# Kernel optimization log

Hardware: AMD Instinct MI355X
Metric: run time of the kernel (lower is better)

## Reference

```python
import jax, jax.numpy as jnp
import numpy as np

HIDDEN = 4096
NH = 32        # query heads
HD = 128       # head dim
NKV = 8        # kv heads
RD = 64        # rotary dim (partial rotary)
THETA = 10000.0
SEQ = 2048


def _rope(x, positions):
    # x: [S, H, HD]; neox-style rope on first RD dims of each head
    half = RD // 2
    inv_freq = 1.0 / (THETA ** (jnp.arange(half, dtype=jnp.float32) / half))
    freqs = positions.astype(jnp.float32)[:, None] * inv_freq[None, :]  # [S, half]
    cos = jnp.cos(freqs)[:, None, :]  # [S,1,half]
    sin = jnp.sin(freqs)[:, None, :]
    x_rot, x_pass = x[..., :RD], x[..., RD:]
    x1, x2 = x_rot[..., :half], x_rot[..., half:]
    o1 = x1 * cos - x2 * sin
    o2 = x2 * cos + x1 * sin
    return jnp.concatenate([o1, o2, x_pass], axis=-1)


def setup_inputs() -> dict:
    key = jax.random.key(0)
    k1, k2, k3 = jax.random.split(key, 3)
    hidden_states = jax.random.normal(k1, (SEQ, HIDDEN), dtype=jnp.float32)
    Wqkv = jax.random.normal(k2, (HIDDEN, (NH + 2 * NKV) * HD), dtype=jnp.float32) * 0.02
    Wo = jax.random.normal(k3, (NH * HD, HIDDEN), dtype=jnp.float32) * 0.02
    positions = jnp.arange(SEQ, dtype=jnp.int64)
    return {"hidden_states": hidden_states, "Wqkv": Wqkv, "Wo": Wo, "positions": positions}


def reference(hidden_states, Wqkv, Wo, positions):
    S = hidden_states.shape[0]
    qkv = hidden_states @ Wqkv  # [S, (NH+2*NKV)*HD]
    q, k, v = jnp.split(qkv, [NH * HD, NH * HD + NKV * HD], axis=-1)
    q = q.reshape(S, NH, HD)
    k = k.reshape(S, NKV, HD)
    v = v.reshape(S, NKV, HD)
    q = _rope(q, positions)
    k = _rope(k, positions)
    # GQA: expand kv heads to query heads
    g = NH // NKV
    k = jnp.repeat(k, g, axis=1)  # [S, NH, HD]
    v = jnp.repeat(v, g, axis=1)
    scale = HD ** -0.5
    scores = jnp.einsum('shd,thd->hst', q, k) * scale  # [NH, S, S]
    causal = jnp.tril(jnp.ones((S, S), dtype=bool))
    scores = jnp.where(causal[None, :, :], scores, jnp.finfo(scores.dtype).min)
    probs = jax.nn.softmax(scores, axis=-1)
    attn = jnp.einsum('hst,thd->shd', probs, v).reshape(S, NH * HD)
    return attn @ Wo
```

## Files before the change

### kernel.cpp

```cpp
#include <hip/hip_runtime.h>

#define S_LEN 2048
#define HID 4096
#define NH 32
#define NKV 8
#define HD 128
#define QKVN 6144
#define KOFF 4096
#define VOFF 5120

typedef unsigned short ushort_t;
typedef unsigned int uint_t;
typedef __attribute__((ext_vector_type(8))) short short8;
typedef __attribute__((ext_vector_type(4))) short short4v;
typedef __attribute__((ext_vector_type(4))) float float4_t;

__device__ __forceinline__ float bf2f(ushort_t u) {
    return __uint_as_float(((uint_t)u) << 16);
}
__device__ __forceinline__ uint_t f2bf(float f) {
    uint_t u = __float_as_uint(f);
    u += 0x7fffu + ((u >> 16) & 1u);
    return u >> 16;
}

__device__ __forceinline__ void gload_lds16(const ushort_t* g, ushort_t* l) {
    __builtin_amdgcn_global_load_lds(
        (const __attribute__((address_space(1))) void*)g,
        (__attribute__((address_space(3))) void*)l, 16, 0, 0);
}

__global__ void f32_to_bf16(const float* __restrict__ in,
                            ushort_t* __restrict__ out) {
    int i = blockIdx.x * 256 + threadIdx.x;
    out[i] = (ushort_t)f2bf(in[i]);
}

__global__ void transpose_f32_bf16(const float* __restrict__ in,
                                   ushort_t* __restrict__ out, int R, int C) {
    __shared__ float t[32][33];
    int c0 = blockIdx.x * 32, r0 = blockIdx.y * 32;
    int ci = threadIdx.x & 31, rb = threadIdx.x >> 5;
#pragma unroll
    for (int p = 0; p < 4; p++) {
        int ri = rb + p * 8;
        t[ri][ci] = in[(size_t)(r0 + ri) * C + c0 + ci];
    }
    __syncthreads();
#pragma unroll
    for (int p = 0; p < 4; p++) {
        int ri = rb + p * 8;
        out[(size_t)(c0 + ri) * R + r0 + ci] = (ushort_t)f2bf(t[ci][ri]);
    }
}

__global__ __launch_bounds__(256, 2)
void gemm_bf16(const ushort_t* __restrict__ A, const ushort_t* __restrict__ BT,
               float* __restrict__ Cout, int M, int N, int K) {
    __shared__ __attribute__((aligned(16))) ushort_t As[128 * 32];
    __shared__ __attribute__((aligned(16))) ushort_t Bs[128 * 32];
    const int tid  = threadIdx.x;
    const int wave = tid >> 6;
    const int lane = tid & 63;
    const int quad = lane >> 4;
    const int l16  = lane & 15;
    const int m0 = blockIdx.y * 128;
    const int n0 = blockIdx.x * 128;
    const int wm = (wave & 1) * 64;
    const int wn = (wave >> 1) * 64;

    const int r0 = tid >> 2;
    const int kc = (tid & 3) * 8;
    const ushort_t* gA0 = A  + (size_t)(m0 + r0)      * K + kc;
    const ushort_t* gA1 = A  + (size_t)(m0 + r0 + 64) * K + kc;
    const ushort_t* gB0 = BT + (size_t)(n0 + r0)      * K + kc;
    const ushort_t* gB1 = BT + (size_t)(n0 + r0 + 64) * K + kc;
    ushort_t* lA0 = &As[r0 * 32 + kc];
    ushort_t* lA1 = lA0 + 64 * 32;
    ushort_t* lB0 = &Bs[r0 * 32 + kc];
    ushort_t* lB1 = lB0 + 64 * 32;

    float4_t acc[4][4] = {};

    for (int k0 = 0; k0 < K; k0 += 32) {
        gload_lds16(gA0 + k0, lA0);
        gload_lds16(gA1 + k0, lA1);
        gload_lds16(gB0 + k0, lB0);
        gload_lds16(gB1 + k0, lB1);
        __syncthreads();

        short8 af[4], bfr[4];
#pragma unroll
        for (int i = 0; i < 4; i++)
            af[i] = *(const short8*)(&As[(wm + i * 16 + l16) * 32 + quad * 8]);
#pragma unroll
        for (int j = 0; j < 4; j++)
            bfr[j] = *(const short8*)(&Bs[(wn + j * 16 + l16) * 32 + quad * 8]);
#pragma unroll
        for (int i = 0; i < 4; i++)
#pragma unroll
            for (int j = 0; j < 4; j++)
                acc[i][j] = __builtin_amdgcn_mfma_f32_16x16x32_bf16(
                    af[i], bfr[j], acc[i][j], 0, 0, 0);
        __syncthreads();
    }

#pragma unroll
    for (int i = 0; i < 4; i++)
#pragma unroll
        for (int j = 0; j < 4; j++)
#pragma unroll
            for (int r = 0; r < 4; r++) {
                int row = m0 + wm + i * 16 + quad * 4 + r;
                int col = n0 + wn + j * 16 + l16;
                Cout[(size_t)row * N + col] = acc[i][j][r];
            }
}

#define QSC 0.12753102543918255f
__global__ void prep_q(const float* __restrict__ qkv, ushort_t* __restrict__ Qb) {
    int idx = blockIdx.x * 256 + threadIdx.x;
    int d = idx & 127;
    int s = (idx >> 7) & 2047;
    int h = idx >> 18;
    const float* row = qkv + (size_t)s * QKVN + h * HD;
    float v;
    if (d < 64) {
        int i = d & 31;
        float invf = exp2f(-(float)i * (13.287712379549449f / 32.0f));
        float fr = (float)s * invf;
        float c, sn;
        sincosf(fr, &sn, &c);
        float x1 = row[i], x2 = row[i + 32];
        v = (d < 32) ? (x1 * c - x2 * sn) : (x2 * c + x1 * sn);
    } else {
        v = row[d];
    }
    Qb[idx] = (ushort_t)f2bf(v * QSC);
}

__global__ void prep_k(const float* __restrict__ qkv, ushort_t* __restrict__ Kb) {
    int idx = blockIdx.x * 256 + threadIdx.x;
    int d = idx & 127;
    int t = (idx >> 7) & 2047;
    int hk = idx >> 18;
    const float* row = qkv + (size_t)t * QKVN + KOFF + hk * HD;
    float v;
    if (d < 64) {
        int i = d & 31;
        float invf = exp2f(-(float)i * (13.287712379549449f / 32.0f));
        float fr = (float)t * invf;
        float c, sn;
        sincosf(fr, &sn, &c);
        float x1 = row[i], x2 = row[i + 32];
        v = (d < 32) ? (x1 * c - x2 * sn) : (x2 * c + x1 * sn);
    } else {
        v = row[d];
    }
    Kb[idx] = (ushort_t)f2bf(v);
}

__global__ void prep_v(const float* __restrict__ qkv, ushort_t* __restrict__ Vt) {
    __shared__ float tile[32][33];
    int hk = blockIdx.z;
    int t0 = blockIdx.x * 32, d0 = blockIdx.y * 32;
    int ci = threadIdx.x & 31, rb = threadIdx.x >> 5;
#pragma unroll
    for (int p = 0; p < 4; p++) {
        int tr = rb + p * 8;
        tile[tr][ci] = qkv[(size_t)(t0 + tr) * QKVN + VOFF + hk * HD + d0 + ci];
    }
    __syncthreads();
#pragma unroll
    for (int p = 0; p < 4; p++) {
        int dr = rb + p * 8;
        Vt[((size_t)hk * HD + d0 + dr) * S_LEN + t0 + ci] = (ushort_t)f2bf(tile[ci][dr]);
    }
}

__global__ __launch_bounds__(256, 4)
void flash_attn(const ushort_t* __restrict__ Qb, const ushort_t* __restrict__ Kb,
                const ushort_t* __restrict__ Vt, ushort_t* __restrict__ attn) {
    __shared__ __attribute__((aligned(16))) ushort_t Ks[2][32 * 128];
    __shared__ __attribute__((aligned(16))) ushort_t Vs[2][128 * 32];

    const int h    = blockIdx.y;
    const int hk   = h >> 2;
    const int tid  = threadIdx.x;
    const int wave = tid >> 6;
    const int lane = tid & 63;
    const int quad = lane >> 4;
    const int l16  = lane & 15;
    const int bx   = 31 - (int)blockIdx.x;
    const int qt   = 4 * bx + wave;
    const int qw   = qt * 16;

    const ushort_t* Qh = Qb + (size_t)h  * S_LEN * HD;
    const ushort_t* Kh = Kb + (size_t)hk * S_LEN * HD;
    const ushort_t* Vh = Vt + (size_t)hk * HD * S_LEN;

    const int krow = tid >> 4;
    const int ksrc = ((tid & 15) ^ (krow & 7)) << 3;
    const ushort_t* gK0 = Kh + (size_t)krow * HD + ksrc;
    const ushort_t* gK1 = Kh + (size_t)(krow + 16) * HD + ksrc;
    const int vrow = tid >> 2;
    const int vtb  = (tid & 3) << 3;
    const ushort_t* gV0 = Vh + (size_t)vrow * S_LEN + vtb;
    const ushort_t* gV1 = Vh + (size_t)(vrow + 64) * S_LEN + vtb;

    ushort_t* lK = &Ks[0][tid * 8];
    ushort_t* lV = &Vs[0][tid * 8];

#define STAGE(buf, t0)                                                        \
    do {                                                                      \
        gload_lds16(gK0 + (size_t)(t0) * HD, lK + (buf) * (32 * 128));        \
        gload_lds16(gK1 + (size_t)(t0) * HD, lK + (buf) * (32 * 128) + 2048); \
        gload_lds16(gV0 + (t0),              lV + (buf) * (128 * 32));        \
        gload_lds16(gV1 + (t0),              lV + (buf) * (128 * 32) + 2048); \
    } while (0)

    short8 qf[4];
#pragma unroll
    for (int c = 0; c < 4; c++)
        qf[c] = *(const short8*)(Qh + (size_t)(qw + l16) * HD + c * 32 + quad * 8);

    float4_t oacc[8] = {};
    float lsum = 0.f;
    const int s0 = (((quad * 2)     & 3) << 4) | l16;
    const int s1 = (((quad * 2 + 1) & 3) << 4) | l16;

    const int T0w   = qw & ~31;
    const int T0max = (16 * (4 * bx + 3)) & ~31;
    const int kxor  = (l16 & 7) << 3;

    STAGE(0, 0);
    __syncthreads();

#pragma unroll 1
    for (int t0 = 0; t0 <= T0max; t0 += 32) {
        const int cur = (t0 >> 5) & 1;
        if (t0 + 32 <= T0max) STAGE(cur ^ 1, t0 + 32);

        const ushort_t* Kbuf = Ks[cur];
        const ushort_t* Vbuf = Vs[cur];

        float4_t stA = {}, stB = {};
#pragma unroll
        for (int c = 0; c < 4; c++) {
            short8 kfA = *(const short8*)(Kbuf + l16 * 128 +
                                          ((c * 32 + quad * 8) ^ kxor));
            short8 kfB = *(const short8*)(Kbuf + (16 + l16) * 128 +
                                          ((c * 32 + quad * 8) ^ kxor));
            stA = __builtin_amdgcn_mfma_f32_16x16x32_bf16(kfA, qf[c], stA, 0, 0, 0);
            stB = __builtin_amdgcn_mfma_f32_16x16x32_bf16(kfB, qf[c], stB, 0, 0, 0);
        }

        const bool maskT = (t0 >= T0w);
        float pA[4], pB[4];
#pragma unroll
        for (int r = 0; r < 4; r++) {
            float eA = exp2f(stA[r]);
            float eB = exp2f(stB[r]);
            if (maskT) {
                int tA = t0 + quad * 4 + r;
                eA = (tA      <= qw + l16) ? eA : 0.f;
                eB = (tA + 16 <= qw + l16) ? eB : 0.f;
            }
            pA[r] = eA; pB[r] = eB;
            lsum += eA + eB;
        }

        uint_t a01 = f2bf(pA[0]) | (f2bf(pA[1]) << 16);
        uint_t a23 = f2bf(pA[2]) | (f2bf(pA[3]) << 16);
        uint_t b01 = f2bf(pB[0]) | (f2bf(pB[1]) << 16);
        uint_t b23 = f2bf(pB[2]) | (f2bf(pB[3]) << 16);
        uint_t A01s0 = (uint_t)__shfl((int)a01, s0);
        uint_t A23s0 = (uint_t)__shfl((int)a23, s0);
        uint_t B01s0 = (uint_t)__shfl((int)b01, s0);
        uint_t B23s0 = (uint_t)__shfl((int)b23, s0);
        uint_t A01s1 = (uint_t)__shfl((int)a01, s1);
        uint_t A23s1 = (uint_t)__shfl((int)a23, s1);
        uint_t B01s1 = (uint_t)__shfl((int)b01, s1);
        uint_t B23s1 = (uint_t)__shfl((int)b23, s1);
        uint_t w[4];
        w[0] = quad < 2 ? A01s0 : B01s0;
        w[1] = quad < 2 ? A23s0 : B23s0;
        w[2] = quad < 2 ? A01s1 : B01s1;
        w[3] = quad < 2 ? A23s1 : B23s1;
        short8 pb;
        __builtin_memcpy(&pb, w, 16);

#pragma unroll
        for (int dt = 0; dt < 8; dt++) {
            short8 vf = *(const short8*)(Vbuf + (dt * 16 + l16) * 32 + quad * 8);
            oacc[dt] = __builtin_amdgcn_mfma_f32_16x16x32_bf16(vf, pb, oacc[dt], 0, 0, 0);
        }

        __syncthreads();
    }
#undef STAGE

    lsum += __shfl_xor(lsum, 16);
    lsum += __shfl_xor(lsum, 32);
    float invl = 1.f / lsum;
    ushort_t* orow = attn + (size_t)(qw + l16) * (NH * HD) + h * HD;
#pragma unroll
    for (int dt = 0; dt < 8; dt++) {
        short4v wv;
#pragma unroll
        for (int r = 0; r < 4; r++)
            wv[r] = (short)f2bf(oacc[dt][r] * invl);
        *(short4v*)(orow + dt * 16 + quad * 4) = wv;
    }
}

extern "C" void kernel_launch(void* const* d_in, const int* in_sizes, int n_in,
                              void* d_out, int out_size, void* d_ws, size_t ws_size,
                              hipStream_t stream) {
    const float* hidden = (const float*)d_in[0];
    const float* Wqkv   = (const float*)d_in[1];
    const float* Wo     = (const float*)d_in[2];
    float* out = (float*)d_out;

    char* ws = (char*)d_ws;
    float*    qkv   = (float*)   (ws);
    ushort_t* attnB = (ushort_t*)(ws);
    ushort_t* hidB  = (ushort_t*)(ws + 50331648);
    ushort_t* Qb    = hidB;
    ushort_t* WqkvT = (ushort_t*)(ws + 67108864);
    ushort_t* WoT   = (ushort_t*)(ws + 117440512);
    ushort_t* Kb    = (ushort_t*)(ws + 150994944);
    ushort_t* Vt    = (ushort_t*)(ws + 155189248);

    f32_to_bf16<<<(S_LEN * HID) / 256, 256, 0, stream>>>(hidden, hidB);
    transpose_f32_bf16<<<dim3(QKVN / 32, HID / 32), 256, 0, stream>>>(Wqkv, WqkvT, HID, QKVN);
    transpose_f32_bf16<<<dim3(HID / 32, HID / 32), 256, 0, stream>>>(Wo, WoT, HID, HID);

    gemm_bf16<<<dim3(QKVN / 128, S_LEN / 128), 256, 0, stream>>>(
        hidB, WqkvT, qkv, S_LEN, QKVN, HID);

    prep_q<<<(NH  * S_LEN * HD) / 256, 256, 0, stream>>>(qkv, Qb);
    prep_k<<<(NKV * S_LEN * HD) / 256, 256, 0, stream>>>(qkv, Kb);
    prep_v<<<dim3(S_LEN / 32, HD / 32, NKV), 256, 0, stream>>>(qkv, Vt);

    flash_attn<<<dim3(32, NH), 256, 0, stream>>>(Qb, Kb, Vt, attnB);

    gemm_bf16<<<dim3(HID / 128, S_LEN / 128), 256, 0, stream>>>(
        attnB, WoT, out, S_LEN, HID, HID);
}
```

Measured before the change: 590.1 us.

## Vectorize conversions, precompute rope table, interleave causal query tiles in attention

Vectorizes the hidden-state bf16 conversion to float4 loads and packs two bf16 values per store in the weight transpose. Adds a cos/sin rope table kernel so prep_q/prep_k stop recomputing sincos per element. Reassigns query tiles in flash attention so each block's waves hold tiles 32 apart, balancing causal work across blocks, and skips tiles beyond each wave's diagonal. The trade-off is that waves within a block now diverge in loop length while still sharing the K/V loads and barriers.

```diff
diff --git a/kernel.cpp b/kernel.cpp
--- a/kernel.cpp
+++ b/kernel.cpp
@@ -30,10 +30,16 @@
         (__attribute__((address_space(3))) void*)l, 16, 0, 0);
 }
 
-__global__ void f32_to_bf16(const float* __restrict__ in,
-                            ushort_t* __restrict__ out) {
+__global__ void f32_to_bf16(const float4* __restrict__ in,
+                            short4v* __restrict__ out) {
     int i = blockIdx.x * 256 + threadIdx.x;
-    out[i] = (ushort_t)f2bf(in[i]);
+    float4 v = in[i];
+    short4v o;
+    o[0] = (short)f2bf(v.x);
+    o[1] = (short)f2bf(v.y);
+    o[2] = (short)f2bf(v.z);
+    o[3] = (short)f2bf(v.w);
+    out[i] = o;
 }
 
 __global__ void transpose_f32_bf16(const float* __restrict__ in,
@@ -47,10 +53,13 @@
         t[ri][ci] = in[(size_t)(r0 + ri) * C + c0 + ci];
     }
     __syncthreads();
-#pragma unroll
-    for (int p = 0; p < 4; p++) {
-        int ri = rb + p * 8;
-        out[(size_t)(c0 + ri) * R + r0 + ci] = (ushort_t)f2bf(t[ci][ri]);
+    int cp = (threadIdx.x & 15) * 2;
+    int rw = threadIdx.x >> 4;
+#pragma unroll
+    for (int p = 0; p < 2; p++) {
+        int ri = rw + p * 16;
+        uint_t w = f2bf(t[cp][ri]) | (f2bf(t[cp + 1][ri]) << 16);
+        *(uint_t*)(&out[(size_t)(c0 + ri) * R + r0 + cp]) = w;
     }
 }
 
@@ -117,8 +126,20 @@
             }
 }
 
+__global__ void rope_tab_k(float2* __restrict__ tab) {
+    int idx = blockIdx.x * 256 + threadIdx.x;
+    int i = idx & 31;
+    int s = idx >> 5;
+    float invf = exp2f(-(float)i * (13.287712379549449f / 32.0f));
+    float fr = (float)s * invf;
+    float c, sn;
+    sincosf(fr, &sn, &c);
+    tab[idx] = make_float2(c, sn);
+}
+
 #define QSC 0.12753102543918255f
-__global__ void prep_q(const float* __restrict__ qkv, ushort_t* __restrict__ Qb) {
+__global__ void prep_q(const float* __restrict__ qkv, const float2* __restrict__ tab,
+                       ushort_t* __restrict__ Qb) {
     int idx = blockIdx.x * 256 + threadIdx.x;
     int d = idx & 127;
     int s = (idx >> 7) & 2047;
@@ -127,19 +148,17 @@
     float v;
     if (d < 64) {
         int i = d & 31;
-        float invf = exp2f(-(float)i * (13.287712379549449f / 32.0f));
-        float fr = (float)s * invf;
-        float c, sn;
-        sincosf(fr, &sn, &c);
+        float2 cs = tab[(s << 5) + i];
         float x1 = row[i], x2 = row[i + 32];
-        v = (d < 32) ? (x1 * c - x2 * sn) : (x2 * c + x1 * sn);
+        v = (d < 32) ? (x1 * cs.x - x2 * cs.y) : (x2 * cs.x + x1 * cs.y);
     } else {
         v = row[d];
     }
     Qb[idx] = (ushort_t)f2bf(v * QSC);
 }
 
-__global__ void prep_k(const float* __restrict__ qkv, ushort_t* __restrict__ Kb) {
+__global__ void prep_k(const float* __restrict__ qkv, const float2* __restrict__ tab,
+                       ushort_t* __restrict__ Kb) {
     int idx = blockIdx.x * 256 + threadIdx.x;
     int d = idx & 127;
     int t = (idx >> 7) & 2047;
@@ -148,12 +167,9 @@
     float v;
     if (d < 64) {
         int i = d & 31;
-        float invf = exp2f(-(float)i * (13.287712379549449f / 32.0f));
-        float fr = (float)t * invf;
-        float c, sn;
-        sincosf(fr, &sn, &c);
+        float2 cs = tab[(t << 5) + i];
         float x1 = row[i], x2 = row[i + 32];
-        v = (d < 32) ? (x1 * c - x2 * sn) : (x2 * c + x1 * sn);
+        v = (d < 32) ? (x1 * cs.x - x2 * cs.y) : (x2 * cs.x + x1 * cs.y);
     } else {
         v = row[d];
     }
@@ -191,8 +207,8 @@
     const int lane = tid & 63;
     const int quad = lane >> 4;
     const int l16  = lane & 15;
-    const int bx   = 31 - (int)blockIdx.x;
-    const int qt   = 4 * bx + wave;
+    const int bx   = (int)blockIdx.x;
+    const int qt   = bx + 32 * wave;
     const int qw   = qt * 16;
 
     const ushort_t* Qh = Qb + (size_t)h  * S_LEN * HD;
@@ -230,7 +246,7 @@
     const int s1 = (((quad * 2 + 1) & 3) << 4) | l16;
 
     const int T0w   = qw & ~31;
-    const int T0max = (16 * (4 * bx + 3)) & ~31;
+    const int T0max = ((bx + 96) * 16) & ~31;
     const int kxor  = (l16 & 7) << 3;
 
     STAGE(0, 0);
@@ -241,59 +257,61 @@
         const int cur = (t0 >> 5) & 1;
         if (t0 + 32 <= T0max) STAGE(cur ^ 1, t0 + 32);
 
-        const ushort_t* Kbuf = Ks[cur];
-        const ushort_t* Vbuf = Vs[cur];
-
-        float4_t stA = {}, stB = {};
-#pragma unroll
-        for (int c = 0; c < 4; c++) {
-            short8 kfA = *(const short8*)(Kbuf + l16 * 128 +
-                                          ((c * 32 + quad * 8) ^ kxor));
-            short8 kfB = *(const short8*)(Kbuf + (16 + l16) * 128 +
-                                          ((c * 32 + quad * 8) ^ kxor));
-            stA = __builtin_amdgcn_mfma_f32_16x16x32_bf16(kfA, qf[c], stA, 0, 0, 0);
-            stB = __builtin_amdgcn_mfma_f32_16x16x32_bf16(kfB, qf[c], stB, 0, 0, 0);
-        }
-
-        const bool maskT = (t0 >= T0w);
-        float pA[4], pB[4];
-#pragma unroll
-        for (int r = 0; r < 4; r++) {
-            float eA = exp2f(stA[r]);
-            float eB = exp2f(stB[r]);
-            if (maskT) {
-                int tA = t0 + quad * 4 + r;
-                eA = (tA      <= qw + l16) ? eA : 0.f;
-                eB = (tA + 16 <= qw + l16) ? eB : 0.f;
+        if (t0 <= T0w) {
+            const ushort_t* Kbuf = Ks[cur];
+            const ushort_t* Vbuf = Vs[cur];
+
+            float4_t stA = {}, stB = {};
+#pragma unroll
+            for (int c = 0; c < 4; c++) {
+                short8 kfA = *(const short8*)(Kbuf + l16 * 128 +
+                                              ((c * 32 + quad * 8) ^ kxor));
+                short8 kfB = *(const short8*)(Kbuf + (16 + l16) * 128 +
+                                              ((c * 32 + quad * 8) ^ kxor));
+                stA = __builtin_amdgcn_mfma_f32_16x16x32_bf16(kfA, qf[c], stA, 0, 0, 0);
+                stB = __builtin_amdgcn_mfma_f32_16x16x32_bf16(kfB, qf[c], stB, 0, 0, 0);
             }
-            pA[r] = eA; pB[r] = eB;
-            lsum += eA + eB;
-        }
-
-        uint_t a01 = f2bf(pA[0]) | (f2bf(pA[1]) << 16);
-        uint_t a23 = f2bf(pA[2]) | (f2bf(pA[3]) << 16);
-        uint_t b01 = f2bf(pB[0]) | (f2bf(pB[1]) << 16);
-        uint_t b23 = f2bf(pB[2]) | (f2bf(pB[3]) << 16);
-        uint_t A01s0 = (uint_t)__shfl((int)a01, s0);
-        uint_t A23s0 = (uint_t)__shfl((int)a23, s0);
-        uint_t B01s0 = (uint_t)__shfl((int)b01, s0);
-        uint_t B23s0 = (uint_t)__shfl((int)b23, s0);
-        uint_t A01s1 = (uint_t)__shfl((int)a01, s1);
-        uint_t A23s1 = (uint_t)__shfl((int)a23, s1);
-        uint_t B01s1 = (uint_t)__shfl((int)b01, s1);
-        uint_t B23s1 = (uint_t)__shfl((int)b23, s1);
-        uint_t w[4];
-        w[0] = quad < 2 ? A01s0 : B01s0;
-        w[1] = quad < 2 ? A23s0 : B23s0;
-        w[2] = quad < 2 ? A01s1 : B01s1;
-        w[3] = quad < 2 ? A23s1 : B23s1;
-        short8 pb;
-        __builtin_memcpy(&pb, w, 16);
-
-#pragma unroll
-        for (int dt = 0; dt < 8; dt++) {
-            short8 vf = *(const short8*)(Vbuf + (dt * 16 + l16) * 32 + quad * 8);
-            oacc[dt] = __builtin_amdgcn_mfma_f32_16x16x32_bf16(vf, pb, oacc[dt], 0, 0, 0);
+
+            const bool maskT = (t0 == T0w);
+            float pA[4], pB[4];
+#pragma unroll
+            for (int r = 0; r < 4; r++) {
+                float eA = exp2f(stA[r]);
+                float eB = exp2f(stB[r]);
+                if (maskT) {
+                    int tA = t0 + quad * 4 + r;
+                    eA = (tA      <= qw + l16) ? eA : 0.f;
+                    eB = (tA + 16 <= qw + l16) ? eB : 0.f;
+                }
+                pA[r] = eA; pB[r] = eB;
+                lsum += eA + eB;
+            }
+
+            uint_t a01 = f2bf(pA[0]) | (f2bf(pA[1]) << 16);
+            uint_t a23 = f2bf(pA[2]) | (f2bf(pA[3]) << 16);
+            uint_t b01 = f2bf(pB[0]) | (f2bf(pB[1]) << 16);
+            uint_t b23 = f2bf(pB[2]) | (f2bf(pB[3]) << 16);
+            uint_t A01s0 = (uint_t)__shfl((int)a01, s0);
+            uint_t A23s0 = (uint_t)__shfl((int)a23, s0);
+            uint_t B01s0 = (uint_t)__shfl((int)b01, s0);
+            uint_t B23s0 = (uint_t)__shfl((int)b23, s0);
+            uint_t A01s1 = (uint_t)__shfl((int)a01, s1);
+            uint_t A23s1 = (uint_t)__shfl((int)a23, s1);
+            uint_t B01s1 = (uint_t)__shfl((int)b01, s1);
+            uint_t B23s1 = (uint_t)__shfl((int)b23, s1);
+            uint_t w[4];
+            w[0] = quad < 2 ? A01s0 : B01s0;
+            w[1] = quad < 2 ? A23s0 : B23s0;
+            w[2] = quad < 2 ? A01s1 : B01s1;
+            w[3] = quad < 2 ? A23s1 : B23s1;
+            short8 pb;
+            __builtin_memcpy(&pb, w, 16);
+
+#pragma unroll
+            for (int dt = 0; dt < 8; dt++) {
+                short8 vf = *(const short8*)(Vbuf + (dt * 16 + l16) * 32 + quad * 8);
+                oacc[dt] = __builtin_amdgcn_mfma_f32_16x16x32_bf16(vf, pb, oacc[dt], 0, 0, 0);
+            }
         }
 
         __syncthreads();
@@ -328,19 +346,22 @@
     ushort_t* hidB  = (ushort_t*)(ws + 50331648);
     ushort_t* Qb    = hidB;
     ushort_t* WqkvT = (ushort_t*)(ws + 67108864);
+    float2*   rtab  = (float2*)  (ws + 67108864);
     ushort_t* WoT   = (ushort_t*)(ws + 117440512);
     ushort_t* Kb    = (ushort_t*)(ws + 150994944);
     ushort_t* Vt    = (ushort_t*)(ws + 155189248);
 
-    f32_to_bf16<<<(S_LEN * HID) / 256, 256, 0, stream>>>(hidden, hidB);
+    f32_to_bf16<<<(S_LEN * HID) / 1024, 256, 0, stream>>>(
+        (const float4*)hidden, (short4v*)hidB);
     transpose_f32_bf16<<<dim3(QKVN / 32, HID / 32), 256, 0, stream>>>(Wqkv, WqkvT, HID, QKVN);
     transpose_f32_bf16<<<dim3(HID / 32, HID / 32), 256, 0, stream>>>(Wo, WoT, HID, HID);
 
     gemm_bf16<<<dim3(QKVN / 128, S_LEN / 128), 256, 0, stream>>>(
         hidB, WqkvT, qkv, S_LEN, QKVN, HID);
 
-    prep_q<<<(NH  * S_LEN * HD) / 256, 256, 0, stream>>>(qkv, Qb);
-    prep_k<<<(NKV * S_LEN * HD) / 256, 256, 0, stream>>>(qkv, Kb);
+    rope_tab_k<<<(S_LEN * 32) / 256, 256, 0, stream>>>(rtab);
+    prep_q<<<(NH  * S_LEN * HD) / 256, 256, 0, stream>>>(qkv, rtab, Qb);
+    prep_k<<<(NKV * S_LEN * HD) / 256, 256, 0, stream>>>(qkv, rtab, Kb);
     prep_v<<<dim3(S_LEN / 32, HD / 32, NKV), 256, 0, stream>>>(qkv, Vt);
 
     flash_attn<<<dim3(32, NH), 256, 0, stream>>>(Qb, Kb, Vt, attnB);
```

After: 561.0 us. 4.9% less time.
